# Kernel tuning notes

Hardware: AMD Instinct MI355X
Metric: run time of the kernel (lower is better)

## Reference

```python
import jax, jax.numpy as jnp
import numpy as np

N_ATOMS = 8192
N_BONDS = 8192
N_ANGLES = 16384
N_DIHEDRALS = 24576


def _chain_idx(key, n, arity):
    # base atom index + consecutive offsets -> guaranteed-distinct atoms per interaction
    base = jax.random.randint(key, (n, 1), 0, N_ATOMS - arity, dtype=jnp.int32)
    return base + jnp.arange(arity, dtype=jnp.int32)[None, :]


def setup_inputs() -> dict:
    key = jax.random.key(0)
    ks = jax.random.split(key, 12)
    positions = jax.random.normal(ks[0], (N_ATOMS, 3), dtype=jnp.float32) * 3.0
    # LJ pair params: strictly-upper-triangular like the original __init__ loops
    triu = jnp.triu(jnp.ones((N_ATOMS, N_ATOMS), dtype=jnp.float32), k=1)
    sigma = jax.random.uniform(ks[1], (N_ATOMS, N_ATOMS), dtype=jnp.float32) * triu
    epsilon = jax.random.uniform(ks[2], (N_ATOMS, N_ATOMS), dtype=jnp.float32) * 0.2 * triu
    bond_idx = _chain_idx(ks[3], N_BONDS, 2)
    k_bond = jax.random.uniform(ks[4], (N_BONDS,), dtype=jnp.float32) * 300.0 + 100.0
    r0 = jax.random.uniform(ks[5], (N_BONDS,), dtype=jnp.float32) + 1.0
    angle_idx = _chain_idx(ks[6], N_ANGLES, 3)
    k_angle = jax.random.uniform(ks[7], (N_ANGLES,), dtype=jnp.float32) * 50.0 + 10.0
    theta0 = jax.random.uniform(ks[8], (N_ANGLES,), dtype=jnp.float32) * 2.0 + 0.5
    dihedral_idx = _chain_idx(ks[9], N_DIHEDRALS, 4)
    k_dihedral = jax.random.uniform(ks[10], (N_DIHEDRALS,), dtype=jnp.float32) * 5.0
    default_phase = jax.random.uniform(ks[11], (N_DIHEDRALS,), dtype=jnp.float32) * np.pi
    n_mult = jax.random.randint(jax.random.fold_in(key, 99), (N_DIHEDRALS,), 1, 4).astype(jnp.float32)
    return {
        "positions": positions,
        "sigma": sigma,
        "epsilon": epsilon,
        "k_bond": k_bond,
        "r0": r0,
        "bond_idx": bond_idx,
        "k_angle": k_angle,
        "theta0": theta0,
        "angle_idx": angle_idx,
        "k_dihedral": k_dihedral,
        "default_phase": default_phase,
        "n_mult": n_mult,
        "dihedral_idx": dihedral_idx,
    }


def _energy(positions, sigma, epsilon, k_bond, r0, bond_idx,
            k_angle, theta0, angle_idx, k_dihedral, default_phase, n_mult, dihedral_idx):
    # pairwise distance map (cdist) + 1e-9, as in get_distance_map
    sq = jnp.sum(positions * positions, axis=-1)  # [N]
    d2 = sq[:, None] + sq[None, :] - 2.0 * (positions @ positions.T)
    dist = jnp.sqrt(jnp.maximum(d2, 0.0)) + 1e-9  # [N, N]

    # bonds: gather pair distances, harmonic energy
    bd = dist[bond_idx[:, 0], bond_idx[:, 1]]
    bond_e = jnp.sum(0.5 * k_bond * (bd - r0) ** 2)

    # angles: acos of normalized dot product
    p1 = positions[angle_idx[:, 0]]
    p2 = positions[angle_idx[:, 1]]
    p3 = positions[angle_idx[:, 2]]
    v1 = p2 - p1
    v2 = p2 - p3
    cos_a = jnp.sum(v1 * v2, axis=-1) / (
        jnp.linalg.norm(v1, axis=1) * jnp.linalg.norm(v2, axis=1))
    ang = jnp.arccos(cos_a)
    angle_e = jnp.sum(0.5 * k_angle * (ang - theta0) ** 2)

    # dihedrals (faithful to the original formulas, including its denominators)
    q1 = positions[dihedral_idx[:, 0]]
    q2 = positions[dihedral_idx[:, 1]]
    q3 = positions[dihedral_idx[:, 2]]
    q4 = positions[dihedral_idx[:, 3]]
    w1 = q2 - q1
    w2 = q3 - q2
    w3 = q4 - q3
    n1 = jnp.cross(w1, w2)
    n2 = jnp.cross(w2, w3)
    cos_d = jnp.sum(n1 * n2, axis=-1) / (
        jnp.linalg.norm(w1, axis=1) * jnp.linalg.norm(w2, axis=1))
    sin_d = jnp.sum(jnp.cross(n1, n2) * w2, axis=-1) / (
        jnp.linalg.norm(w2, axis=1) * jnp.linalg.norm(n1, axis=1) * jnp.linalg.norm(n2, axis=1))
    dih = jnp.arctan2(sin_d, cos_d)
    dihedral_e = jnp.sum(0.5 * k_dihedral * (1.0 + jnp.cos(n_mult * dih - default_phase)))

    # Lennard-Jones over dense NxN pair matrices
    r6 = (sigma / dist) ** 6
    r12 = r6 * r6
    lj_e = jnp.sum(4.0 * epsilon * (r12 - r6))

    # NOTE: original forward computes coulomb but does NOT add it to total_energy
    return bond_e + angle_e + dihedral_e + lj_e


def reference(positions, sigma, epsilon, k_bond, r0, bond_idx,
              k_angle, theta0, angle_idx, k_dihedral, default_phase, n_mult, dihedral_idx):
    return _energy(positions, sigma, epsilon, k_bond, r0, bond_idx,
                   k_angle, theta0, angle_idx, k_dihedral, default_phase, n_mult, dihedral_idx)
```

## Files before the change

kernel.cpp:

```cpp
#include <hip/hip_runtime.h>

#define NATOMS   8192
#define NVEC     (NATOMS / 4)
#define BT       256
#define NB_LJ    NATOMS
#define NBONDS   8192
#define NANGLES  16384
#define NDIH     24576
#define NB_BOND  ((NBONDS + NANGLES + NDIH) / BT)

__device__ __forceinline__ float sq_np(float x, float y, float z)
{
    return __fadd_rn(__fadd_rn(__fmul_rn(x, x), __fmul_rn(y, y)),
                     __fmul_rn(z, z));
}

__device__ __forceinline__ float lj_chunk(const float* __restrict__ srow,
                                          const float* __restrict__ erow,
                                          const float* __restrict__ pos,
                                          float xi, float yi, float zi,
                                          float sqi, int v)
{
    const float4 s4 = *reinterpret_cast<const float4*>(srow + 4 * v);
    const float4 e4 = *reinterpret_cast<const float4*>(erow + 4 * v);
    const float4 p0 = *reinterpret_cast<const float4*>(pos + 12 * v + 0);
    const float4 p1 = *reinterpret_cast<const float4*>(pos + 12 * v + 4);
    const float4 p2 = *reinterpret_cast<const float4*>(pos + 12 * v + 8);

    const float px[4] = { p0.x, p0.w, p1.z, p2.y };
    const float py[4] = { p0.y, p1.x, p1.w, p2.z };
    const float pz[4] = { p0.z, p1.y, p2.x, p2.w };
    const float ss[4] = { s4.x, s4.y, s4.z, s4.w };
    const float ee[4] = { e4.x, e4.y, e4.z, e4.w };

    float acc = 0.0f;
    #pragma unroll
    for (int k = 0; k < 4; ++k) {
        float t = __fmul_rn(xi, px[k]);
        t = fmaf(yi, py[k], t);
        t = fmaf(zi, pz[k], t);
        const float sqj = sq_np(px[k], py[k], pz[k]);
        const float d2  = __fsub_rn(__fadd_rn(sqi, sqj),
                                    __fmul_rn(2.0f, t));
        const float dist  = __fadd_rn(__fsqrt_rn(fmaxf(d2, 0.0f)), 1e-9f);
        const float ratio = __fdiv_rn(ss[k], dist);
        const float r2  = __fmul_rn(ratio, ratio);
        const float r6  = __fmul_rn(__fmul_rn(r2, r2), r2);
        const float r12 = __fmul_rn(r6, r6);
        acc += 4.0f * ee[k] * (r12 - r6);
    }
    return acc;
}

__global__ __launch_bounds__(BT)
void lj_kernel(const float* __restrict__ pos,
               const float* __restrict__ sigma,
               const float* __restrict__ eps,
               float* __restrict__ partial)
{
    const int i   = blockIdx.x;
    const int tid = threadIdx.x;

    const float xi = pos[3 * i + 0];
    const float yi = pos[3 * i + 1];
    const float zi = pos[3 * i + 2];
    const float sqi = sq_np(xi, yi, zi);

    const float* __restrict__ srow = sigma + (size_t)i * NATOMS;
    const float* __restrict__ erow = eps   + (size_t)i * NATOMS;

    float acc = 0.0f;
    const int v0 = (i + 1) >> 2;

    for (int v = v0 + tid; v < NVEC; v += 2 * BT) {
        acc += lj_chunk(srow, erow, pos, xi, yi, zi, sqi, v);
        const int v2 = v + BT;
        if (v2 < NVEC)
            acc += lj_chunk(srow, erow, pos, xi, yi, zi, sqi, v2);
    }

    #pragma unroll
    for (int off = 32; off > 0; off >>= 1)
        acc += __shfl_down(acc, off, 64);
    __shared__ float red[BT / 64];
    if ((tid & 63) == 0) red[tid >> 6] = acc;
    __syncthreads();
    if (tid == 0)
        partial[i] = red[0] + red[1] + red[2] + red[3];
}

__global__ __launch_bounds__(BT)
void bonded_kernel(const float* __restrict__ pos,
                   const float* __restrict__ k_bond,
                   const float* __restrict__ r0,
                   const int*   __restrict__ bidx,
                   const float* __restrict__ k_angle,
                   const float* __restrict__ th0,
                   const int*   __restrict__ aidx,
                   const float* __restrict__ k_dih,
                   const float* __restrict__ phase,
                   const float* __restrict__ nmult,
                   const int*   __restrict__ didx,
                   float* __restrict__ partial)
{
    const int t = blockIdx.x * BT + threadIdx.x;
    float e = 0.0f;

    if (t < NBONDS) {
        const int a = bidx[2 * t + 0];
        const int b = bidx[2 * t + 1];
        const float xa = pos[3 * a + 0], ya = pos[3 * a + 1], za = pos[3 * a + 2];
        const float xb = pos[3 * b + 0], yb = pos[3 * b + 1], zb = pos[3 * b + 2];
        float dt2 = __fmul_rn(xa, xb);
        dt2 = fmaf(ya, yb, dt2);
        dt2 = fmaf(za, zb, dt2);
        const float d2 = __fsub_rn(__fadd_rn(sq_np(xa, ya, za), sq_np(xb, yb, zb)),
                                   __fmul_rn(2.0f, dt2));
        const float d  = __fadd_rn(__fsqrt_rn(fmaxf(d2, 0.0f)), 1e-9f);
        const float dd = d - r0[t];
        e = 0.5f * k_bond[t] * dd * dd;
    } else if (t < NBONDS + NANGLES) {
        const int u = t - NBONDS;
        const int a = aidx[3 * u + 0];
        const int b = aidx[3 * u + 1];
        const int c = aidx[3 * u + 2];
        const float v1x = pos[3 * b + 0] - pos[3 * a + 0];
        const float v1y = pos[3 * b + 1] - pos[3 * a + 1];
        const float v1z = pos[3 * b + 2] - pos[3 * a + 2];
        const float v2x = pos[3 * b + 0] - pos[3 * c + 0];
        const float v2y = pos[3 * b + 1] - pos[3 * c + 1];
        const float v2z = pos[3 * b + 2] - pos[3 * c + 2];
        const float dot = fmaf(v1x, v2x, fmaf(v1y, v2y, v1z * v2z));
        const float n1  = sqrtf(fmaf(v1x, v1x, fmaf(v1y, v1y, v1z * v1z)));
        const float n2  = sqrtf(fmaf(v2x, v2x, fmaf(v2y, v2y, v2z * v2z)));
        float ca = dot / (n1 * n2);
        ca = fminf(1.0f, fmaxf(-1.0f, ca));
        const float ang = acosf(ca);
        const float dth = ang - th0[u];
        e = 0.5f * k_angle[u] * dth * dth;
    } else {
        const int u = t - NBONDS - NANGLES;
        const int a = didx[4 * u + 0];
        const int b = didx[4 * u + 1];
        const int c = didx[4 * u + 2];
        const int d = didx[4 * u + 3];
        const float w1x = pos[3 * b + 0] - pos[3 * a + 0];
        const float w1y = pos[3 * b + 1] - pos[3 * a + 1];
        const float w1z = pos[3 * b + 2] - pos[3 * a + 2];
        const float w2x = pos[3 * c + 0] - pos[3 * b + 0];
        const float w2y = pos[3 * c + 1] - pos[3 * b + 1];
        const float w2z = pos[3 * c + 2] - pos[3 * b + 2];
        const float w3x = pos[3 * d + 0] - pos[3 * c + 0];
        const float w3y = pos[3 * d + 1] - pos[3 * c + 1];
        const float w3z = pos[3 * d + 2] - pos[3 * c + 2];
        const float n1x = w1y * w2z - w1z * w2y;
        const float n1y = w1z * w2x - w1x * w2z;
        const float n1z = w1x * w2y - w1y * w2x;
        const float n2x = w2y * w3z - w2z * w3y;
        const float n2y = w2z * w3x - w2x * w3z;
        const float n2z = w2x * w3y - w2y * w3x;
        const float dot12 = fmaf(n1x, n2x, fmaf(n1y, n2y, n1z * n2z));
        const float nw1 = sqrtf(fmaf(w1x, w1x, fmaf(w1y, w1y, w1z * w1z)));
        const float nw2 = sqrtf(fmaf(w2x, w2x, fmaf(w2y, w2y, w2z * w2z)));
        const float nn1 = sqrtf(fmaf(n1x, n1x, fmaf(n1y, n1y, n1z * n1z)));
        const float nn2 = sqrtf(fmaf(n2x, n2x, fmaf(n2y, n2y, n2z * n2z)));
        const float cos_d = dot12 / (nw1 * nw2);
        const float cx = n1y * n2z - n1z * n2y;
        const float cy = n1z * n2x - n1x * n2z;
        const float cz = n1x * n2y - n1y * n2x;
        const float sden = nw2 * nn1 * nn2;
        const float sin_d = fmaf(cx, w2x, fmaf(cy, w2y, cz * w2z)) / sden;
        const float dih = atan2f(sin_d, cos_d);
        e = 0.5f * k_dih[u] * (1.0f + cosf(nmult[u] * dih - phase[u]));
    }

    #pragma unroll
    for (int off = 32; off > 0; off >>= 1)
        e += __shfl_down(e, off, 64);
    __shared__ float red[BT / 64];
    if ((threadIdx.x & 63) == 0) red[threadIdx.x >> 6] = e;
    __syncthreads();
    if (threadIdx.x == 0)
        partial[NB_LJ + blockIdx.x] = red[0] + red[1] + red[2] + red[3];
}

#define RT 1024
__global__ __launch_bounds__(RT)
void reduce_kernel(const float* __restrict__ partial, int n,
                   float* __restrict__ out)
{
    double s = 0.0;
    for (int i = threadIdx.x; i < n; i += RT)
        s += (double)partial[i];
    #pragma unroll
    for (int off = 32; off > 0; off >>= 1)
        s += __shfl_down(s, off, 64);
    __shared__ double red[RT / 64];
    if ((threadIdx.x & 63) == 0) red[threadIdx.x >> 6] = s;
    __syncthreads();
    if (threadIdx.x == 0) {
        double t = 0.0;
        #pragma unroll
        for (int w = 0; w < RT / 64; ++w) t += red[w];
        out[0] = (float)t;
    }
}

extern "C" void kernel_launch(void* const* d_in, const int* in_sizes, int n_in,
                              void* d_out, int out_size, void* d_ws, size_t ws_size,
                              hipStream_t stream)
{
    const float* pos   = (const float*)d_in[0];
    const float* sigma = (const float*)d_in[1];
    const float* eps   = (const float*)d_in[2];
    const float* kb    = (const float*)d_in[3];
    const float* r0    = (const float*)d_in[4];
    const int*   bidx  = (const int*)  d_in[5];
    const float* ka    = (const float*)d_in[6];
    const float* th0   = (const float*)d_in[7];
    const int*   aidx  = (const int*)  d_in[8];
    const float* kd    = (const float*)d_in[9];
    const float* ph    = (const float*)d_in[10];
    const float* nm    = (const float*)d_in[11];
    const int*   didx  = (const int*)  d_in[12];

    float* ws  = (float*)d_ws;
    float* out = (float*)d_out;

    lj_kernel<<<NB_LJ, BT, 0, stream>>>(pos, sigma, eps, ws);
    bonded_kernel<<<NB_BOND, BT, 0, stream>>>(pos, kb, r0, bidx, ka, th0, aidx,
                                              kd, ph, nm, didx, ws);
    reduce_kernel<<<1, RT, 0, stream>>>(ws, NB_LJ + NB_BOND, out);
}
```

Measured before the change: 55.27 us.

## Fold bonded energy terms into single-block final reduction kernel

Removes the separate bonded kernel launch and computes all 49152 bond, angle and dihedral terms inside the one-block reduction kernel, which also sums the LJ partials. This saves a kernel launch and the partial writes for the bonded terms. The cost is that the bonded work, including acosf, atan2f and cosf, now runs serially on one workgroup of 1024 threads, about 48 iterations per thread, instead of being spread across 192 blocks. The LJ loop is also restructured so the paired-chunk bounds check is hoisted into a tail step.

```diff
diff --git a/kernel.cpp b/kernel.cpp
--- a/kernel.cpp
+++ b/kernel.cpp
@@ -7,7 +7,7 @@
 #define NBONDS   8192
 #define NANGLES  16384
 #define NDIH     24576
-#define NB_BOND  ((NBONDS + NANGLES + NDIH) / BT)
+#define NBONDED  (NBONDS + NANGLES + NDIH)
 
 __device__ __forceinline__ float sq_np(float x, float y, float z)
 {
@@ -72,12 +72,13 @@
     float acc = 0.0f;
     const int v0 = (i + 1) >> 2;
 
-    for (int v = v0 + tid; v < NVEC; v += 2 * BT) {
+    int v = v0 + tid;
+    for (; v + BT < NVEC; v += 2 * BT) {
         acc += lj_chunk(srow, erow, pos, xi, yi, zi, sqi, v);
-        const int v2 = v + BT;
-        if (v2 < NVEC)
-            acc += lj_chunk(srow, erow, pos, xi, yi, zi, sqi, v2);
-    }
+        acc += lj_chunk(srow, erow, pos, xi, yi, zi, sqi, v + BT);
+    }
+    if (v < NVEC)
+        acc += lj_chunk(srow, erow, pos, xi, yi, zi, sqi, v);
 
     #pragma unroll
     for (int off = 32; off > 0; off >>= 1)
@@ -89,116 +90,107 @@
         partial[i] = red[0] + red[1] + red[2] + red[3];
 }
 
-__global__ __launch_bounds__(BT)
-void bonded_kernel(const float* __restrict__ pos,
-                   const float* __restrict__ k_bond,
-                   const float* __restrict__ r0,
-                   const int*   __restrict__ bidx,
-                   const float* __restrict__ k_angle,
-                   const float* __restrict__ th0,
-                   const int*   __restrict__ aidx,
-                   const float* __restrict__ k_dih,
-                   const float* __restrict__ phase,
-                   const float* __restrict__ nmult,
-                   const int*   __restrict__ didx,
-                   float* __restrict__ partial)
-{
-    const int t = blockIdx.x * BT + threadIdx.x;
-    float e = 0.0f;
-
-    if (t < NBONDS) {
-        const int a = bidx[2 * t + 0];
-        const int b = bidx[2 * t + 1];
-        const float xa = pos[3 * a + 0], ya = pos[3 * a + 1], za = pos[3 * a + 2];
-        const float xb = pos[3 * b + 0], yb = pos[3 * b + 1], zb = pos[3 * b + 2];
-        float dt2 = __fmul_rn(xa, xb);
-        dt2 = fmaf(ya, yb, dt2);
-        dt2 = fmaf(za, zb, dt2);
-        const float d2 = __fsub_rn(__fadd_rn(sq_np(xa, ya, za), sq_np(xb, yb, zb)),
-                                   __fmul_rn(2.0f, dt2));
-        const float d  = __fadd_rn(__fsqrt_rn(fmaxf(d2, 0.0f)), 1e-9f);
-        const float dd = d - r0[t];
-        e = 0.5f * k_bond[t] * dd * dd;
-    } else if (t < NBONDS + NANGLES) {
-        const int u = t - NBONDS;
-        const int a = aidx[3 * u + 0];
-        const int b = aidx[3 * u + 1];
-        const int c = aidx[3 * u + 2];
-        const float v1x = pos[3 * b + 0] - pos[3 * a + 0];
-        const float v1y = pos[3 * b + 1] - pos[3 * a + 1];
-        const float v1z = pos[3 * b + 2] - pos[3 * a + 2];
-        const float v2x = pos[3 * b + 0] - pos[3 * c + 0];
-        const float v2y = pos[3 * b + 1] - pos[3 * c + 1];
-        const float v2z = pos[3 * b + 2] - pos[3 * c + 2];
-        const float dot = fmaf(v1x, v2x, fmaf(v1y, v2y, v1z * v2z));
-        const float n1  = sqrtf(fmaf(v1x, v1x, fmaf(v1y, v1y, v1z * v1z)));
-        const float n2  = sqrtf(fmaf(v2x, v2x, fmaf(v2y, v2y, v2z * v2z)));
-        float ca = dot / (n1 * n2);
-        ca = fminf(1.0f, fmaxf(-1.0f, ca));
-        const float ang = acosf(ca);
-        const float dth = ang - th0[u];
-        e = 0.5f * k_angle[u] * dth * dth;
-    } else {
-        const int u = t - NBONDS - NANGLES;
-        const int a = didx[4 * u + 0];
-        const int b = didx[4 * u + 1];
-        const int c = didx[4 * u + 2];
-        const int d = didx[4 * u + 3];
-        const float w1x = pos[3 * b + 0] - pos[3 * a + 0];
-        const float w1y = pos[3 * b + 1] - pos[3 * a + 1];
-        const float w1z = pos[3 * b + 2] - pos[3 * a + 2];
-        const float w2x = pos[3 * c + 0] - pos[3 * b + 0];
-        const float w2y = pos[3 * c + 1] - pos[3 * b + 1];
-        const float w2z = pos[3 * c + 2] - pos[3 * b + 2];
-        const float w3x = pos[3 * d + 0] - pos[3 * c + 0];
-        const float w3y = pos[3 * d + 1] - pos[3 * c + 1];
-        const float w3z = pos[3 * d + 2] - pos[3 * c + 2];
-        const float n1x = w1y * w2z - w1z * w2y;
-        const float n1y = w1z * w2x - w1x * w2z;
-        const float n1z = w1x * w2y - w1y * w2x;
-        const float n2x = w2y * w3z - w2z * w3y;
-        const float n2y = w2z * w3x - w2x * w3z;
-        const float n2z = w2x * w3y - w2y * w3x;
-        const float dot12 = fmaf(n1x, n2x, fmaf(n1y, n2y, n1z * n2z));
-        const float nw1 = sqrtf(fmaf(w1x, w1x, fmaf(w1y, w1y, w1z * w1z)));
-        const float nw2 = sqrtf(fmaf(w2x, w2x, fmaf(w2y, w2y, w2z * w2z)));
-        const float nn1 = sqrtf(fmaf(n1x, n1x, fmaf(n1y, n1y, n1z * n1z)));
-        const float nn2 = sqrtf(fmaf(n2x, n2x, fmaf(n2y, n2y, n2z * n2z)));
-        const float cos_d = dot12 / (nw1 * nw2);
-        const float cx = n1y * n2z - n1z * n2y;
-        const float cy = n1z * n2x - n1x * n2z;
-        const float cz = n1x * n2y - n1y * n2x;
-        const float sden = nw2 * nn1 * nn2;
-        const float sin_d = fmaf(cx, w2x, fmaf(cy, w2y, cz * w2z)) / sden;
-        const float dih = atan2f(sin_d, cos_d);
-        e = 0.5f * k_dih[u] * (1.0f + cosf(nmult[u] * dih - phase[u]));
-    }
-
-    #pragma unroll
-    for (int off = 32; off > 0; off >>= 1)
-        e += __shfl_down(e, off, 64);
-    __shared__ float red[BT / 64];
-    if ((threadIdx.x & 63) == 0) red[threadIdx.x >> 6] = e;
-    __syncthreads();
-    if (threadIdx.x == 0)
-        partial[NB_LJ + blockIdx.x] = red[0] + red[1] + red[2] + red[3];
-}
-
 #define RT 1024
 __global__ __launch_bounds__(RT)
-void reduce_kernel(const float* __restrict__ partial, int n,
-                   float* __restrict__ out)
-{
+void tail_kernel(const float* __restrict__ pos,
+                 const float* __restrict__ k_bond,
+                 const float* __restrict__ r0,
+                 const int*   __restrict__ bidx,
+                 const float* __restrict__ k_angle,
+                 const float* __restrict__ th0,
+                 const int*   __restrict__ aidx,
+                 const float* __restrict__ k_dih,
+                 const float* __restrict__ phase,
+                 const float* __restrict__ nmult,
+                 const int*   __restrict__ didx,
+                 const float* __restrict__ partial,
+                 float* __restrict__ out)
+{
+    const int tid = threadIdx.x;
     double s = 0.0;
-    for (int i = threadIdx.x; i < n; i += RT)
-        s += (double)partial[i];
+
+    for (int t = tid; t < NBONDED; t += RT) {
+        float e;
+        if (t < NBONDS) {
+            const int a = bidx[2 * t + 0];
+            const int b = bidx[2 * t + 1];
+            const float xa = pos[3 * a + 0], ya = pos[3 * a + 1], za = pos[3 * a + 2];
+            const float xb = pos[3 * b + 0], yb = pos[3 * b + 1], zb = pos[3 * b + 2];
+            float dt2 = __fmul_rn(xa, xb);
+            dt2 = fmaf(ya, yb, dt2);
+            dt2 = fmaf(za, zb, dt2);
+            const float d2 = __fsub_rn(__fadd_rn(sq_np(xa, ya, za), sq_np(xb, yb, zb)),
+                                       __fmul_rn(2.0f, dt2));
+            const float d  = __fadd_rn(__fsqrt_rn(fmaxf(d2, 0.0f)), 1e-9f);
+            const float dd = d - r0[t];
+            e = 0.5f * k_bond[t] * dd * dd;
+        } else if (t < NBONDS + NANGLES) {
+            const int u = t - NBONDS;
+            const int a = aidx[3 * u + 0];
+            const int b = aidx[3 * u + 1];
+            const int c = aidx[3 * u + 2];
+            const float v1x = pos[3 * b + 0] - pos[3 * a + 0];
+            const float v1y = pos[3 * b + 1] - pos[3 * a + 1];
+            const float v1z = pos[3 * b + 2] - pos[3 * a + 2];
+            const float v2x = pos[3 * b + 0] - pos[3 * c + 0];
+            const float v2y = pos[3 * b + 1] - pos[3 * c + 1];
+            const float v2z = pos[3 * b + 2] - pos[3 * c + 2];
+            const float dot = fmaf(v1x, v2x, fmaf(v1y, v2y, v1z * v2z));
+            const float n1  = sqrtf(fmaf(v1x, v1x, fmaf(v1y, v1y, v1z * v1z)));
+            const float n2  = sqrtf(fmaf(v2x, v2x, fmaf(v2y, v2y, v2z * v2z)));
+            float ca = dot / (n1 * n2);
+            ca = fminf(1.0f, fmaxf(-1.0f, ca));
+            const float ang = acosf(ca);
+            const float dth = ang - th0[u];
+            e = 0.5f * k_angle[u] * dth * dth;
+        } else {
+            const int u = t - NBONDS - NANGLES;
+            const int a = didx[4 * u + 0];
+            const int b = didx[4 * u + 1];
+            const int c = didx[4 * u + 2];
+            const int d = didx[4 * u + 3];
+            const float w1x = pos[3 * b + 0] - pos[3 * a + 0];
+            const float w1y = pos[3 * b + 1] - pos[3 * a + 1];
+            const float w1z = pos[3 * b + 2] - pos[3 * a + 2];
+            const float w2x = pos[3 * c + 0] - pos[3 * b + 0];
+            const float w2y = pos[3 * c + 1] - pos[3 * b + 1];
+            const float w2z = pos[3 * c + 2] - pos[3 * b + 2];
+            const float w3x = pos[3 * d + 0] - pos[3 * c + 0];
+            const float w3y = pos[3 * d + 1] - pos[3 * c + 1];
+            const float w3z = pos[3 * d + 2] - pos[3 * c + 2];
+            const float n1x = w1y * w2z - w1z * w2y;
+            const float n1y = w1z * w2x - w1x * w2z;
+            const float n1z = w1x * w2y - w1y * w2x;
+            const float n2x = w2y * w3z - w2z * w3y;
+            const float n2y = w2z * w3x - w2x * w3z;
+            const float n2z = w2x * w3y - w2y * w3x;
+            const float dot12 = fmaf(n1x, n2x, fmaf(n1y, n2y, n1z * n2z));
+            const float nw1 = sqrtf(fmaf(w1x, w1x, fmaf(w1y, w1y, w1z * w1z)));
+            const float nw2 = sqrtf(fmaf(w2x, w2x, fmaf(w2y, w2y, w2z * w2z)));
+            const float nn1 = sqrtf(fmaf(n1x, n1x, fmaf(n1y, n1y, n1z * n1z)));
+            const float nn2 = sqrtf(fmaf(n2x, n2x, fmaf(n2y, n2y, n2z * n2z)));
+            const float cos_d = dot12 / (nw1 * nw2);
+            const float cx = n1y * n2z - n1z * n2y;
+            const float cy = n1z * n2x - n1x * n2z;
+            const float cz = n1x * n2y - n1y * n2x;
+            const float sden = nw2 * nn1 * nn2;
+            const float sin_d = fmaf(cx, w2x, fmaf(cy, w2y, cz * w2z)) / sden;
+            const float dih = atan2f(sin_d, cos_d);
+            e = 0.5f * k_dih[u] * (1.0f + cosf(nmult[u] * dih - phase[u]));
+        }
+        s += (double)e;
+    }
+
+    for (int p = tid; p < NB_LJ; p += RT)
+        s += (double)partial[p];
+
     #pragma unroll
     for (int off = 32; off > 0; off >>= 1)
         s += __shfl_down(s, off, 64);
     __shared__ double red[RT / 64];
-    if ((threadIdx.x & 63) == 0) red[threadIdx.x >> 6] = s;
+    if ((tid & 63) == 0) red[tid >> 6] = s;
     __syncthreads();
-    if (threadIdx.x == 0) {
+    if (tid == 0) {
         double t = 0.0;
         #pragma unroll
         for (int w = 0; w < RT / 64; ++w) t += red[w];
@@ -228,7 +220,6 @@
     float* out = (float*)d_out;
 
     lj_kernel<<<NB_LJ, BT, 0, stream>>>(pos, sigma, eps, ws);
-    bonded_kernel<<<NB_BOND, BT, 0, stream>>>(pos, kb, r0, bidx, ka, th0, aidx,
-                                              kd, ph, nm, didx, ws);
-    reduce_kernel<<<1, RT, 0, stream>>>(ws, NB_LJ + NB_BOND, out);
-}
+    tail_kernel<<<1, RT, 0, stream>>>(pos, kb, r0, bidx, ka, th0, aidx,
+                                      kd, ph, nm, didx, ws, out);
+}
```

After: 206.9 us. 3.74x slower.
